# Optimization experiments

Hardware: AMD Instinct MI355X
Metric: run time of the kernel (lower is better)

## Reference

```python
import jax, jax.numpy as jnp
import numpy as np

NQ = 8
NL = 6
DIM = 2 ** NQ
C64 = jnp.complex64
I2 = jnp.eye(2, dtype=C64)
PX = jnp.array([[0., 1.], [1., 0.]], dtype=C64)
PY = jnp.array([[0., -1j], [1j, 0.]], dtype=C64)
PZ = jnp.array([[1., 0.], [0., -1.]], dtype=C64)
# sign of Pauli-Z eigenvalue for each computational basis state, wires 0..3 (wire 0 = MSB)
_idx = np.arange(DIM)
_SIGNS = jnp.asarray(np.stack([1.0 - 2.0 * ((_idx >> (NQ - 1 - w)) & 1) for w in range(4)]).astype(np.float32))  # (4, 256)

def _rot(t, P):
    # exp(-i t/2 P) = cos(t/2) I - i sin(t/2) P
    th = t.astype(jnp.float32) / 2
    return jnp.cos(th) * I2 - 1j * jnp.sin(th) * P

def _apply1(st, U, w):
    # apply 2x2 unitary U on wire w; st: (B, 2,2,...,2)
    s = jnp.moveaxis(st, w + 1, -1)
    return jnp.moveaxis(s @ U.T, -1, w + 1)

def _cnot(st, c, t):
    # flip target axis where control bit == 1
    s = jnp.moveaxis(st, (c + 1, t + 1), (1, 2))
    s = jnp.concatenate([s[:, :1], s[:, 1:, ::-1]], axis=1)
    return jnp.moveaxis(s, (1, 2), (c + 1, t + 1))

def _quantum(x, weights):
    B = x.shape[0]
    # AmplitudeEmbedding with normalize=True
    psi = (x / jnp.linalg.norm(x, axis=1, keepdims=True)).astype(C64)
    st = psi.reshape((B,) + (2,) * NQ)
    for l in range(NL):
        lw = weights[l]
        for q in range(NQ):
            st = _apply1(st, _rot(lw[3 * q], PX), q)
            st = _apply1(st, _rot(lw[3 * q + 1], PY), q)
            st = _apply1(st, _rot(lw[3 * q + 2], PZ), q)
        for i in range(NQ - 1):
            st = _cnot(st, i, i + 1)
        st = _cnot(st, NQ - 1, 0)
        for i in range(0, NQ, 2):
            if i + 2 < NQ:
                st = _cnot(st, i, i + 2)
    probs = jnp.abs(st.reshape(B, DIM)) ** 2
    return probs @ _SIGNS.T  # (B, 4) Z expectations on wires 0..3

def _bn(h, g, b):
    # BatchNorm1d, training mode (batch statistics, biased variance)
    m = h.mean(0)
    v = h.var(0)
    return g * (h - m) * jax.lax.rsqrt(v + 1e-5) + b

def _forward(x, q_weights, aW, ab, fW1, fb1, fW2, fb2, cW1, cb1, g1, be1, cW2, cb2, g2, be2, cW3, cb3, cW4, cb4):
    q = _quantum(x, q_weights)                     # (B, 4)
    qf = q @ aW.T + ab                             # quantum_adapter
    cf = jnp.tanh(jax.nn.relu(x @ fW1.T + fb1) @ fW2.T + fb2)  # feature_processor
    h = qf + cf
    h = jax.nn.relu(_bn(h @ cW1.T + cb1, g1, be1))
    h = jax.nn.relu(_bn(h @ cW2.T + cb2, g2, be2))
    h = jax.nn.relu(h @ cW3.T + cb3)
    return jax.nn.sigmoid(h @ cW4.T + cb4)         # (B, 1)

def setup_inputs():
    key = jax.random.key(0)
    ks = jax.random.split(key, 21)
    f32 = jnp.float32
    r = lambda k, shp, s: jax.random.normal(k, shp, dtype=f32) * s
    B = 8192
    return {
        'x': r(ks[0], (B, 256), 1.0),
        'q_weights': r(ks[1], (NL, NQ * 3), 1.0),
        'aW': r(ks[2], (4, 4), 0.5), 'ab': r(ks[3], (4,), 0.1),
        'fW1': r(ks[4], (64, 256), 0.0625), 'fb1': r(ks[5], (64,), 0.05),
        'fW2': r(ks[6], (4, 64), 0.125), 'fb2': r(ks[7], (4,), 0.05),
        'cW1': r(ks[8], (32, 4), 0.5), 'cb1': r(ks[9], (32,), 0.05),
        'g1': 1.0 + r(ks[10], (32,), 0.05), 'be1': r(ks[11], (32,), 0.05),
        'cW2': r(ks[12], (16, 32), 0.18), 'cb2': r(ks[13], (16,), 0.05),
        'g2': 1.0 + r(ks[14], (16,), 0.05), 'be2': r(ks[15], (16,), 0.05),
        'cW3': r(ks[16], (8, 16), 0.25), 'cb3': r(ks[17], (8,), 0.05),
        'cW4': r(ks[18], (1, 8), 0.35), 'cb4': r(ks[19], (1,), 0.05),
    }

def reference(x, q_weights, aW, ab, fW1, fb1, fW2, fb2, cW1, cb1, g1, be1, cW2, cb2, g2, be2, cW3, cb3, cW4, cb4):
    return _forward(x, q_weights, aW, ab, fW1, fb1, fW2, fb2, cW1, cb1, g1, be1, cW2, cb2, g2, be2, cW3, cb3, cW4, cb4)
```

## Files before the change

### kernel.cpp

```cpp
#include <hip/hip_runtime.h>
#include <math.h>

#define INV_B (1.0f / 8192.0f)

typedef float  v2f  __attribute__((ext_vector_type(2)));
typedef _Float16 half8 __attribute__((ext_vector_type(8)));
typedef float  f32x4 __attribute__((ext_vector_type(4)));

struct QTables {
    int xm[6][8];
    int rm[6][8];
    int meas[4];
};
constexpr QTables make_tables() {
    QTables T{};
    int Mrow[8] = {}, Ncol[8] = {};
    for (int b = 0; b < 8; ++b) { Mrow[b] = 1 << b; Ncol[b] = 1 << b; }
    constexpr int bc[11] = {7,6,5,4,3,2,1,0,7,5,3};
    constexpr int bt[11] = {6,5,4,3,2,1,0,7,5,3,1};
    for (int l = 0; l < 6; ++l) {
        for (int w = 0; w < 8; ++w) { T.xm[l][w] = Ncol[7 - w]; T.rm[l][w] = Mrow[7 - w]; }
        for (int k = 0; k < 11; ++k) { Mrow[bt[k]] ^= Mrow[bc[k]]; Ncol[bc[k]] ^= Ncol[bt[k]]; }
    }
    for (int w = 0; w < 4; ++w) T.meas[w] = Mrow[7 - w];
    return T;
}
constexpr QTables TB = make_tables();

template<int ML>
static __device__ __forceinline__ float lanex(float v) {
    if constexpr (ML == 0) { return v; }
    else if constexpr (ML == 1) { return __int_as_float(__builtin_amdgcn_update_dpp(0, __float_as_int(v), 0xB1, 0xF, 0xF, true)); }
    else if constexpr (ML == 2) { return __int_as_float(__builtin_amdgcn_update_dpp(0, __float_as_int(v), 0x4E, 0xF, 0xF, true)); }
    else if constexpr (ML == 3) { return __int_as_float(__builtin_amdgcn_update_dpp(0, __float_as_int(v), 0x1B, 0xF, 0xF, true)); }
    else if constexpr (ML < 32) { return __int_as_float(__builtin_amdgcn_ds_swizzle(__float_as_int(v), 0x1F | (ML << 10))); }
    else { return __shfl_xor(v, ML, 64); }
}

static __device__ __forceinline__ float tanh_fast(float v) {
    const float c = fminf(fmaxf(v, -10.f), 10.f);
    const float e = __expf(2.f * c);
    return (e - 1.f) / (e + 1.f);
}

template<int XM, int RM>
static __device__ __forceinline__ void gate(v2f (&z)[4], const int lane,
                                            const float u00r, const float u00i,
                                            const float u01r, const float u01i) {
    constexpr int ML = XM >> 2, MR = XM & 3;
    constexpr int RL = RM >> 2, RR = RM & 3;
    const int pl = __popc(lane & RL) & 1;
    const float csi0 = pl ? -u00i : u00i;
    const float cpr0 = pl ? -u01r : u01r;
    const float csi1 = -csi0, cpr1 = -cpr0;
    v2f p[4];
    #pragma unroll
    for (int r = 0; r < 4; ++r) {
        p[r].x = lanex<ML>(z[r ^ MR].x);
        p[r].y = lanex<ML>(z[r ^ MR].y);
    }
    #pragma unroll
    for (int r = 0; r < 4; ++r) {
        const int pb = __builtin_popcount(r & RR) & 1;
        const float csi = pb ? csi1 : csi0;
        const float cpr = pb ? cpr1 : cpr0;
        const v2f zs = { -z[r].y, z[r].x };
        const v2f ps = { -p[r].y, p[r].x };
        z[r] = ((u00r * z[r] + csi * zs) + cpr * p[r]) + u01i * ps;
    }
}

#define XS 264
__global__ __launch_bounds__(256) void k_pre(
        const float* __restrict__ x, const float* __restrict__ qw,
        const float* __restrict__ fW1, const float* __restrict__ fb1,
        const float* __restrict__ fW2, const float* __restrict__ fb2,
        _Float16* __restrict__ Wt, float* __restrict__ cfws,
        float* __restrict__ accz) {
    const int t = threadIdx.x, b = blockIdx.x;

    if (b >= 128) {
        __shared__ float4 Us[48];
        if (t < 48) {
            const int l = t >> 3, q = t & 7;
            const float* a = qw + l * 24 + q * 3;
            const float h1 = 0.5f * a[0], h2 = 0.5f * a[1], h3 = 0.5f * a[2];
            const float c1 = cosf(h1), s1 = sinf(h1);
            const float c2 = cosf(h2), s2 = sinf(h2);
            const float c3 = cosf(h3), s3 = sinf(h3);
            const float m00r =  c1 * c2, m00i =  s1 * s2;
            const float m01r = -c1 * s2, m01i = -s1 * c2;
            float4 u;
            u.x = m00r * c3 + m00i * s3;  u.y = m00i * c3 - m00r * s3;
            u.z = m01r * c3 + m01i * s3;  u.w = m01i * c3 - m01r * s3;
            Us[t] = u;
        }
        __syncthreads();
        const int lane = t & 63, wv = t >> 6;
        const int k = (b - 128) * 4 + wv;
        v2f z[4];
        #pragma unroll
        for (int r = 0; r < 4; ++r) {
            z[r].x = (4 * lane + r == k) ? 1.f : 0.f;
            z[r].y = 0.f;
        }
#define GATE(L, W) { const float4 u = Us[(L) * 8 + (W)]; \
                     gate<TB.xm[L][W], TB.rm[L][W]>(z, lane, u.x, u.y, u.z, u.w); }
#define LAYER(L) GATE(L,0) GATE(L,1) GATE(L,2) GATE(L,3) GATE(L,4) GATE(L,5) GATE(L,6) GATE(L,7)
        LAYER(0) LAYER(1) LAYER(2) LAYER(3) LAYER(4) LAYER(5)
#undef LAYER
#undef GATE
        #pragma unroll
        for (int r = 0; r < 4; ++r) {
            const int i = 4 * lane + r;
            Wt[(long)i * 256 + k]         = (_Float16)z[r].x;
            Wt[(long)(256 + i) * 256 + k] = (_Float16)z[r].y;
        }
        return;
    }

    if (t < 16) accz[b * 16 + t] = 0.f;

    __shared__ _Float16 xl[64 * XS];
    __shared__ _Float16 wl[64 * XS];
    const long r0 = (long)b * 64;
    #pragma unroll
    for (int i = 0; i < 16; ++i) {
        const int idx = i * 256 + t;
        const int row = idx >> 6, c4 = idx & 63;
        const float4 xv = ((const float4*)(x + (r0 + row) * 256))[c4];
        _Float16* d = &xl[row * XS + c4 * 4];
        d[0] = (_Float16)xv.x; d[1] = (_Float16)xv.y;
        d[2] = (_Float16)xv.z; d[3] = (_Float16)xv.w;
        const float4 wv2 = ((const float4*)(fW1 + (long)row * 256))[c4];
        _Float16* e = &wl[row * XS + c4 * 4];
        e[0] = (_Float16)wv2.x; e[1] = (_Float16)wv2.y;
        e[2] = (_Float16)wv2.z; e[3] = (_Float16)wv2.w;
    }
    __syncthreads();

    const int lane = t & 63, w4 = t >> 6;
    const int g = lane >> 4, col = lane & 15;
    const int rloc = w4 * 16 + col;

    half8 bf[8];
    #pragma unroll
    for (int kb = 0; kb < 8; ++kb)
        bf[kb] = *(const half8*)&xl[rloc * XS + kb * 32 + g * 8];

    float accc[4] = {0.f, 0.f, 0.f, 0.f};
    #pragma unroll
    for (int jc = 0; jc < 4; ++jc) {
        f32x4 cv = {0.f, 0.f, 0.f, 0.f};
        #pragma unroll
        for (int kb = 0; kb < 8; ++kb) {
            const half8 af = *(const half8*)&wl[(jc * 16 + col) * XS + kb * 32 + g * 8];
            cv = __builtin_amdgcn_mfma_f32_16x16x32_f16(af, bf[kb], cv, 0, 0, 0);
        }
        #pragma unroll
        for (int r = 0; r < 4; ++r) {
            const int j = jc * 16 + g * 4 + r;
            const float z = fmaxf(cv[r] + fb1[j], 0.f);
            #pragma unroll
            for (int c = 0; c < 4; ++c) accc[c] += z * fW2[c * 64 + j];
        }
    }
    #pragma unroll
    for (int c = 0; c < 4; ++c) {
        accc[c] += __shfl_xor(accc[c], 16, 64);
        accc[c] += __shfl_xor(accc[c], 32, 64);
    }
    if (g == 0) {
        float4 o;
        o.x = tanh_fast(accc[0] + fb2[0]);
        o.y = tanh_fast(accc[1] + fb2[1]);
        o.z = tanh_fast(accc[2] + fb2[2]);
        o.w = tanh_fast(accc[3] + fb2[3]);
        ((float4*)cfws)[r0 + w4 * 16 + col] = o;
    }
}

__global__ __launch_bounds__(128) void k_gemm(
        const float* __restrict__ x, const _Float16* __restrict__ Wt,
        const float* __restrict__ cfws,
        const float* __restrict__ aW, const float* __restrict__ ab,
        float* __restrict__ hws, float* __restrict__ acc1) {
    const int t = threadIdx.x;
    const int lane = t & 63, w = t >> 6;
    const int col = lane & 15, quad = lane >> 4;
    const int R0 = blockIdx.x * 32;

    __shared__ _Float16 xa[32 * XS];
    #pragma unroll
    for (int i = 0; i < 16; ++i) {
        const int idx = i * 128 + t;
        const int row = idx >> 6, c4 = idx & 63;
        const float4 xv = ((const float4*)(x + (long)(R0 + row) * 256))[c4];
        _Float16* d = &xa[row * XS + c4 * 4];
        d[0] = (_Float16)xv.x; d[1] = (_Float16)xv.y;
        d[2] = (_Float16)xv.z; d[3] = (_Float16)xv.w;
    }
    __syncthreads();

    half8 af[8];
    #pragma unroll
    for (int kb = 0; kb < 8; ++kb)
        af[kb] = *(const half8*)&xa[(w * 16 + col) * XS + kb * 32 + quad * 8];

    int slm[4];
    #pragma unroll
    for (int mw = 0; mw < 4; ++mw) slm[mw] = __popc(col & TB.meas[mw]) & 1;

    float sS[4] = {0.f, 0.f, 0.f, 0.f};
    float sq[4][4] = {{0.f}};
    const _Float16* bre = Wt + (long)col * 256;
    const _Float16* bim = Wt + (long)(256 + col) * 256;

    #pragma unroll
    for (int c = 0; c < 16; ++c) {
        f32x4 cr0 = {0.f,0.f,0.f,0.f}, cr1 = {0.f,0.f,0.f,0.f};
        f32x4 ci0 = {0.f,0.f,0.f,0.f}, ci1 = {0.f,0.f,0.f,0.f};
        const long rowoff = (long)(c * 16) * 256 + quad * 8;
        #pragma unroll
        for (int kb = 0; kb < 4; ++kb) {
            const half8 br = *(const half8*)(bre + rowoff + kb * 32);
            cr0 = __builtin_amdgcn_mfma_f32_16x16x32_f16(af[kb], br, cr0, 0, 0, 0);
            const half8 bi = *(const half8*)(bim + rowoff + kb * 32);
            ci0 = __builtin_amdgcn_mfma_f32_16x16x32_f16(af[kb], bi, ci0, 0, 0, 0);
            const half8 br2 = *(const half8*)(bre + rowoff + (kb + 4) * 32);
            cr1 = __builtin_amdgcn_mfma_f32_16x16x32_f16(af[kb + 4], br2, cr1, 0, 0, 0);
            const half8 bi2 = *(const half8*)(bim + rowoff + (kb + 4) * 32);
            ci1 = __builtin_amdgcn_mfma_f32_16x16x32_f16(af[kb + 4], bi2, ci1, 0, 0, 0);
        }
        float sgn[4];
        #pragma unroll
        for (int mw = 0; mw < 4; ++mw) {
            const int scw = __builtin_popcount((c * 16) & TB.meas[mw]) & 1;
            sgn[mw] = (slm[mw] ^ scw) ? -1.f : 1.f;
        }
        #pragma unroll
        for (int r = 0; r < 4; ++r) {
            const float re = cr0[r] + cr1[r], im = ci0[r] + ci1[r];
            const float p = re * re + im * im;
            sS[r] += p;
            #pragma unroll
            for (int mw = 0; mw < 4; ++mw) sq[mw][r] = fmaf(sgn[mw], p, sq[mw][r]);
        }
    }

    #pragma unroll
    for (int r = 0; r < 4; ++r) {
        sS[r] += lanex<1>(sS[r]); sS[r] += lanex<2>(sS[r]);
        sS[r] += lanex<4>(sS[r]); sS[r] += lanex<8>(sS[r]);
        #pragma unroll
        for (int mw = 0; mw < 4; ++mw) {
            sq[mw][r] += lanex<1>(sq[mw][r]); sq[mw][r] += lanex<2>(sq[mw][r]);
            sq[mw][r] += lanex<4>(sq[mw][r]); sq[mw][r] += lanex<8>(sq[mw][r]);
        }
    }

    __shared__ float hb[32][4];
    if (col == 0) {
        #pragma unroll
        for (int r = 0; r < 4; ++r) {
            const int mloc = w * 16 + quad * 4 + r;
            const int row = R0 + mloc;
            const float inv = 1.0f / sS[r];
            float qe[4];
            #pragma unroll
            for (int mw = 0; mw < 4; ++mw) qe[mw] = sq[mw][r] * inv;
            const float4 cfv = ((const float4*)cfws)[row];
            const float cf[4] = {cfv.x, cfv.y, cfv.z, cfv.w};
            float h[4];
            #pragma unroll
            for (int kk = 0; kk < 4; ++kk) {
                float s = ab[kk] + cf[kk];
                #pragma unroll
                for (int j = 0; j < 4; ++j) s += aW[kk * 4 + j] * qe[j];
                h[kk] = s;
            }
            ((float4*)hws)[row] = make_float4(h[0], h[1], h[2], h[3]);
            hb[mloc][0] = h[0]; hb[mloc][1] = h[1];
            hb[mloc][2] = h[2]; hb[mloc][3] = h[3];
        }
    }
    __syncthreads();
    if (t < 20) {
        const int j = (t - 4) >> 2, kk = (t - 4) & 3;
        float v = 0.f;
        for (int rr = 0; rr < 32; ++rr)
            v += (t < 4) ? hb[rr][t] : hb[rr][j] * hb[rr][kk];
        atomicAdd(acc1 + (blockIdx.x & 31) * 20 + t, v);
    }
}

__global__ __launch_bounds__(64) void k_mid(
        const float* __restrict__ hws, const float* __restrict__ acc1,
        const float* __restrict__ cW1, const float* __restrict__ cb1,
        const float* __restrict__ g1, const float* __restrict__ be1,
        const float* __restrict__ cW2, const float* __restrict__ cb2,
        float* __restrict__ z2ws, float* __restrict__ acc2) {
    const int t = threadIdx.x;
    __shared__ float sA[20];
    __shared__ float m1s[32], is1[32];
    if (t < 20) {
        float s = 0.f;
        for (int sl = 0; sl < 32; ++sl) s += acc1[sl * 20 + t];
        sA[t] = s;
    }
    __syncthreads();
    if (t < 32) {
        float mu[4], w[4];
        #pragma unroll
        for (int k = 0; k < 4; ++k) mu[k] = sA[k] * INV_B;
        float m = cb1[t];
        #pragma unroll
        for (int k = 0; k < 4; ++k) { w[k] = cW1[t * 4 + k]; m += w[k] * mu[k]; }
        float var = 0.f;
        #pragma unroll
        for (int a2 = 0; a2 < 4; ++a2)
            #pragma unroll
            for (int b2 = 0; b2 < 4; ++b2)
                var += w[a2] * w[b2] * (sA[4 + a2 * 4 + b2] * INV_B - mu[a2] * mu[b2]);
        m1s[t] = m;
        is1[t] = 1.0f / sqrtf(var + 1e-5f);
    }
    __syncthreads();

    const long e = (long)blockIdx.x * 64 + t;
    const float4 h4 = ((const float4*)hws)[e];
    const float h[4] = {h4.x, h4.y, h4.z, h4.w};
    float a1[32];
    #pragma unroll
    for (int j = 0; j < 32; ++j) {
        float zz = cb1[j];
        #pragma unroll
        for (int k = 0; k < 4; ++k) zz += cW1[j * 4 + k] * h[k];
        a1[j] = fmaxf((zz - m1s[j]) * is1[j] * g1[j] + be1[j], 0.f);
    }
    float z2[16];
    #pragma unroll
    for (int k = 0; k < 16; ++k) {
        float s = cb2[k];
        #pragma unroll
        for (int j = 0; j < 32; ++j) s += cW2[k * 32 + j] * a1[j];
        z2[k] = s;
    }
    float4* zp = (float4*)(z2ws + e * 16);
    zp[0] = make_float4(z2[0], z2[1], z2[2], z2[3]);
    zp[1] = make_float4(z2[4], z2[5], z2[6], z2[7]);
    zp[2] = make_float4(z2[8], z2[9], z2[10], z2[11]);
    zp[3] = make_float4(z2[12], z2[13], z2[14], z2[15]);

    float sv[16], sq2[16];
    #pragma unroll
    for (int k = 0; k < 16; ++k) { sv[k] = z2[k]; sq2[k] = z2[k] * z2[k]; }
    #pragma unroll
    for (int m = 1; m < 64; m <<= 1) {
        #pragma unroll
        for (int k = 0; k < 16; ++k) {
            sv[k] += __shfl_xor(sv[k], m, 64);
            sq2[k] += __shfl_xor(sq2[k], m, 64);
        }
    }
    if (t == 0) {
        float* dst = acc2 + ((int)blockIdx.x & 31) * 32;
        #pragma unroll
        for (int k = 0; k < 16; ++k) atomicAdd(dst + k, sv[k]);
        #pragma unroll
        for (int k = 0; k < 16; ++k) atomicAdd(dst + 16 + k, sq2[k]);
    }
}

__global__ __launch_bounds__(64) void k_out(
        const float* __restrict__ z2ws, const float* __restrict__ acc2,
        const float* __restrict__ g2, const float* __restrict__ be2,
        const float* __restrict__ cW3, const float* __restrict__ cb3,
        const float* __restrict__ cW4, const float* __restrict__ cb4,
        float* __restrict__ out) {
    const int t = threadIdx.x;
    __shared__ float sB[32];
    __shared__ float m2s[16], is2[16];
    if (t < 32) {
        float s = 0.f;
        for (int sl = 0; sl < 32; ++sl) s += acc2[sl * 32 + t];
        sB[t] = s;
    }
    __syncthreads();
    if (t < 16) {
        const float m = sB[t] * INV_B;
        const float var = sB[16 + t] * INV_B - m * m;
        m2s[t] = m;
        is2[t] = 1.0f / sqrtf(var + 1e-5f);
    }
    __syncthreads();

    const long e = (long)blockIdx.x * 64 + t;
    const float4* zp = (const float4*)(z2ws + e * 16);
    const float4 v0 = zp[0], v1 = zp[1], v2 = zp[2], v3 = zp[3];
    const float z2[16] = {v0.x, v0.y, v0.z, v0.w, v1.x, v1.y, v1.z, v1.w,
                          v2.x, v2.y, v2.z, v2.w, v3.x, v3.y, v3.z, v3.w};
    float a2[16];
    #pragma unroll
    for (int k = 0; k < 16; ++k)
        a2[k] = fmaxf((z2[k] - m2s[k]) * is2[k] * g2[k] + be2[k], 0.f);
    float z3[8];
    #pragma unroll
    for (int j = 0; j < 8; ++j) {
        float s = cb3[j];
        #pragma unroll
        for (int k = 0; k < 16; ++k) s += cW3[j * 16 + k] * a2[k];
        z3[j] = fmaxf(s, 0.f);
    }
    float y = cb4[0];
    #pragma unroll
    for (int j = 0; j < 8; ++j) y += cW4[j] * z3[j];
    out[e] = 1.0f / (1.0f + expf(-y));
}

extern "C" void kernel_launch(void* const* d_in, const int* in_sizes, int n_in,
                              void* d_out, int out_size, void* d_ws, size_t ws_size,
                              hipStream_t stream) {
    (void)in_sizes; (void)n_in; (void)out_size; (void)ws_size;
    const float* x   = (const float*)d_in[0];
    const float* qw  = (const float*)d_in[1];
    const float* aW  = (const float*)d_in[2];
    const float* ab  = (const float*)d_in[3];
    const float* fW1 = (const float*)d_in[4];
    const float* fb1 = (const float*)d_in[5];
    const float* fW2 = (const float*)d_in[6];
    const float* fb2 = (const float*)d_in[7];
    const float* cW1 = (const float*)d_in[8];
    const float* cb1 = (const float*)d_in[9];
    const float* g1  = (const float*)d_in[10];
    const float* be1 = (const float*)d_in[11];
    const float* cW2 = (const float*)d_in[12];
    const float* cb2 = (const float*)d_in[13];
    const float* g2  = (const float*)d_in[14];
    const float* be2 = (const float*)d_in[15];
    const float* cW3 = (const float*)d_in[16];
    const float* cb3 = (const float*)d_in[17];
    const float* cW4 = (const float*)d_in[18];
    const float* cb4 = (const float*)d_in[19];

    float* ws   = (float*)d_ws;
    float* acc1 = ws;
    float* acc2 = ws + 1024;
    float* cfws = ws + 4096;
    float* hws  = ws + 40960;
    float* z2ws = ws + 81920;
    _Float16* Wt = (_Float16*)(ws + 215040);

    k_pre <<<192, 256, 0, stream>>>(x, qw, fW1, fb1, fW2, fb2, Wt, cfws, ws);
    k_gemm<<<256, 128, 0, stream>>>(x, Wt, cfws, aW, ab, hws, acc1);
    k_mid <<<128, 64, 0, stream>>>(hws, acc1, cW1, cb1, g1, be1, cW2, cb2, z2ws, acc2);
    k_out <<<128, 64, 0, stream>>>(z2ws, acc2, g2, be2, cW3, cb3, cW4, cb4, (float*)d_out);
}
```

Before: 137.7 us.

## Fuse feature MLP into quantum GEMM and merge tail kernels via grid barrier

The classical feature MLP (x·fW1, relu, fW2, tanh) moves out of the prelude kernel and into the main GEMM kernel, which reuses the fp16 x fragments already staged in LDS. The prelude now only builds the circuit unitary and an fp16 copy of fW1, so the second read of x and the cf workspace round-trip go away. The mid and output kernels are merged into one kernel that uses an atomic counter spin-barrier for the second BatchNorm statistics, dropping the z2 workspace and one launch. The spin barrier assumes all 128 blocks are resident at once, and the counter is zeroed only by the prelude's accumulator clear.

```diff
diff --git a/kernel.cpp b/kernel.cpp
--- a/kernel.cpp
+++ b/kernel.cpp
@@ -70,119 +70,59 @@
     }
 }
 
-#define XS 264
 __global__ __launch_bounds__(256) void k_pre(
-        const float* __restrict__ x, const float* __restrict__ qw,
-        const float* __restrict__ fW1, const float* __restrict__ fb1,
-        const float* __restrict__ fW2, const float* __restrict__ fb2,
-        _Float16* __restrict__ Wt, float* __restrict__ cfws,
+        const float* __restrict__ qw, const float* __restrict__ fW1,
+        _Float16* __restrict__ Wt, _Float16* __restrict__ fW1h,
         float* __restrict__ accz) {
     const int t = threadIdx.x, b = blockIdx.x;
-
-    if (b >= 128) {
-        __shared__ float4 Us[48];
-        if (t < 48) {
-            const int l = t >> 3, q = t & 7;
-            const float* a = qw + l * 24 + q * 3;
-            const float h1 = 0.5f * a[0], h2 = 0.5f * a[1], h3 = 0.5f * a[2];
-            const float c1 = cosf(h1), s1 = sinf(h1);
-            const float c2 = cosf(h2), s2 = sinf(h2);
-            const float c3 = cosf(h3), s3 = sinf(h3);
-            const float m00r =  c1 * c2, m00i =  s1 * s2;
-            const float m01r = -c1 * s2, m01i = -s1 * c2;
-            float4 u;
-            u.x = m00r * c3 + m00i * s3;  u.y = m00i * c3 - m00r * s3;
-            u.z = m01r * c3 + m01i * s3;  u.w = m01i * c3 - m01r * s3;
-            Us[t] = u;
-        }
-        __syncthreads();
-        const int lane = t & 63, wv = t >> 6;
-        const int k = (b - 128) * 4 + wv;
-        v2f z[4];
-        #pragma unroll
-        for (int r = 0; r < 4; ++r) {
-            z[r].x = (4 * lane + r == k) ? 1.f : 0.f;
-            z[r].y = 0.f;
-        }
+    const int e = b * 256 + t;
+    fW1h[e] = (_Float16)fW1[e];
+    if (t < 32) accz[b * 32 + t] = 0.f;
+
+    __shared__ float4 Us[48];
+    if (t < 48) {
+        const int l = t >> 3, q = t & 7;
+        const float* a = qw + l * 24 + q * 3;
+        const float h1 = 0.5f * a[0], h2 = 0.5f * a[1], h3 = 0.5f * a[2];
+        const float c1 = cosf(h1), s1 = sinf(h1);
+        const float c2 = cosf(h2), s2 = sinf(h2);
+        const float c3 = cosf(h3), s3 = sinf(h3);
+        const float m00r =  c1 * c2, m00i =  s1 * s2;
+        const float m01r = -c1 * s2, m01i = -s1 * c2;
+        float4 u;
+        u.x = m00r * c3 + m00i * s3;  u.y = m00i * c3 - m00r * s3;
+        u.z = m01r * c3 + m01i * s3;  u.w = m01i * c3 - m01r * s3;
+        Us[t] = u;
+    }
+    __syncthreads();
+    const int lane = t & 63, wv = t >> 6;
+    const int k = b * 4 + wv;
+    v2f z[4];
+    #pragma unroll
+    for (int r = 0; r < 4; ++r) {
+        z[r].x = (4 * lane + r == k) ? 1.f : 0.f;
+        z[r].y = 0.f;
+    }
 #define GATE(L, W) { const float4 u = Us[(L) * 8 + (W)]; \
                      gate<TB.xm[L][W], TB.rm[L][W]>(z, lane, u.x, u.y, u.z, u.w); }
 #define LAYER(L) GATE(L,0) GATE(L,1) GATE(L,2) GATE(L,3) GATE(L,4) GATE(L,5) GATE(L,6) GATE(L,7)
-        LAYER(0) LAYER(1) LAYER(2) LAYER(3) LAYER(4) LAYER(5)
+    LAYER(0) LAYER(1) LAYER(2) LAYER(3) LAYER(4) LAYER(5)
 #undef LAYER
 #undef GATE
-        #pragma unroll
-        for (int r = 0; r < 4; ++r) {
-            const int i = 4 * lane + r;
-            Wt[(long)i * 256 + k]         = (_Float16)z[r].x;
-            Wt[(long)(256 + i) * 256 + k] = (_Float16)z[r].y;
-        }
-        return;
-    }
-
-    if (t < 16) accz[b * 16 + t] = 0.f;
-
-    __shared__ _Float16 xl[64 * XS];
-    __shared__ _Float16 wl[64 * XS];
-    const long r0 = (long)b * 64;
-    #pragma unroll
-    for (int i = 0; i < 16; ++i) {
-        const int idx = i * 256 + t;
-        const int row = idx >> 6, c4 = idx & 63;
-        const float4 xv = ((const float4*)(x + (r0 + row) * 256))[c4];
-        _Float16* d = &xl[row * XS + c4 * 4];
-        d[0] = (_Float16)xv.x; d[1] = (_Float16)xv.y;
-        d[2] = (_Float16)xv.z; d[3] = (_Float16)xv.w;
-        const float4 wv2 = ((const float4*)(fW1 + (long)row * 256))[c4];
-        _Float16* e = &wl[row * XS + c4 * 4];
-        e[0] = (_Float16)wv2.x; e[1] = (_Float16)wv2.y;
-        e[2] = (_Float16)wv2.z; e[3] = (_Float16)wv2.w;
-    }
-    __syncthreads();
-
-    const int lane = t & 63, w4 = t >> 6;
-    const int g = lane >> 4, col = lane & 15;
-    const int rloc = w4 * 16 + col;
-
-    half8 bf[8];
-    #pragma unroll
-    for (int kb = 0; kb < 8; ++kb)
-        bf[kb] = *(const half8*)&xl[rloc * XS + kb * 32 + g * 8];
-
-    float accc[4] = {0.f, 0.f, 0.f, 0.f};
-    #pragma unroll
-    for (int jc = 0; jc < 4; ++jc) {
-        f32x4 cv = {0.f, 0.f, 0.f, 0.f};
-        #pragma unroll
-        for (int kb = 0; kb < 8; ++kb) {
-            const half8 af = *(const half8*)&wl[(jc * 16 + col) * XS + kb * 32 + g * 8];
-            cv = __builtin_amdgcn_mfma_f32_16x16x32_f16(af, bf[kb], cv, 0, 0, 0);
-        }
-        #pragma unroll
-        for (int r = 0; r < 4; ++r) {
-            const int j = jc * 16 + g * 4 + r;
-            const float z = fmaxf(cv[r] + fb1[j], 0.f);
-            #pragma unroll
-            for (int c = 0; c < 4; ++c) accc[c] += z * fW2[c * 64 + j];
-        }
-    }
-    #pragma unroll
-    for (int c = 0; c < 4; ++c) {
-        accc[c] += __shfl_xor(accc[c], 16, 64);
-        accc[c] += __shfl_xor(accc[c], 32, 64);
-    }
-    if (g == 0) {
-        float4 o;
-        o.x = tanh_fast(accc[0] + fb2[0]);
-        o.y = tanh_fast(accc[1] + fb2[1]);
-        o.z = tanh_fast(accc[2] + fb2[2]);
-        o.w = tanh_fast(accc[3] + fb2[3]);
-        ((float4*)cfws)[r0 + w4 * 16 + col] = o;
-    }
-}
-
+    #pragma unroll
+    for (int r = 0; r < 4; ++r) {
+        const int i = 4 * lane + r;
+        Wt[(long)i * 256 + k]         = (_Float16)z[r].x;
+        Wt[(long)(256 + i) * 256 + k] = (_Float16)z[r].y;
+    }
+}
+
+#define XS 264
 __global__ __launch_bounds__(128) void k_gemm(
         const float* __restrict__ x, const _Float16* __restrict__ Wt,
-        const float* __restrict__ cfws,
+        const _Float16* __restrict__ fW1h,
+        const float* __restrict__ fb1, const float* __restrict__ fW2,
+        const float* __restrict__ fb2,
         const float* __restrict__ aW, const float* __restrict__ ab,
         float* __restrict__ hws, float* __restrict__ acc1) {
     const int t = threadIdx.x;
@@ -206,6 +146,36 @@
     #pragma unroll
     for (int kb = 0; kb < 8; ++kb)
         af[kb] = *(const half8*)&xa[(w * 16 + col) * XS + kb * 32 + quad * 8];
+
+    float sc[4][4] = {{0.f}};
+    #pragma unroll
+    for (int jt = 0; jt < 4; ++jt) {
+        const int j = jt * 16 + col;
+        f32x4 mv = {0.f, 0.f, 0.f, 0.f};
+        #pragma unroll
+        for (int kb = 0; kb < 8; ++kb) {
+            const half8 bw = *(const half8*)(fW1h + (long)j * 256 + kb * 32 + quad * 8);
+            mv = __builtin_amdgcn_mfma_f32_16x16x32_f16(af[kb], bw, mv, 0, 0, 0);
+        }
+        const float b1 = fb1[j];
+        const float w20 = fW2[j], w21 = fW2[64 + j];
+        const float w22 = fW2[128 + j], w23 = fW2[192 + j];
+        #pragma unroll
+        for (int r = 0; r < 4; ++r) {
+            const float z1 = fmaxf(mv[r] + b1, 0.f);
+            sc[0][r] = fmaf(z1, w20, sc[0][r]);
+            sc[1][r] = fmaf(z1, w21, sc[1][r]);
+            sc[2][r] = fmaf(z1, w22, sc[2][r]);
+            sc[3][r] = fmaf(z1, w23, sc[3][r]);
+        }
+    }
+    #pragma unroll
+    for (int c = 0; c < 4; ++c)
+        #pragma unroll
+        for (int r = 0; r < 4; ++r) {
+            sc[c][r] += lanex<1>(sc[c][r]); sc[c][r] += lanex<2>(sc[c][r]);
+            sc[c][r] += lanex<4>(sc[c][r]); sc[c][r] += lanex<8>(sc[c][r]);
+        }
 
     int slm[4];
     #pragma unroll
@@ -247,7 +217,6 @@
             for (int mw = 0; mw < 4; ++mw) sq[mw][r] = fmaf(sgn[mw], p, sq[mw][r]);
         }
     }
-
     #pragma unroll
     for (int r = 0; r < 4; ++r) {
         sS[r] += lanex<1>(sS[r]); sS[r] += lanex<2>(sS[r]);
@@ -266,11 +235,11 @@
             const int mloc = w * 16 + quad * 4 + r;
             const int row = R0 + mloc;
             const float inv = 1.0f / sS[r];
-            float qe[4];
+            float qe[4], cf[4];
             #pragma unroll
             for (int mw = 0; mw < 4; ++mw) qe[mw] = sq[mw][r] * inv;
-            const float4 cfv = ((const float4*)cfws)[row];
-            const float cf[4] = {cfv.x, cfv.y, cfv.z, cfv.w};
+            #pragma unroll
+            for (int c = 0; c < 4; ++c) cf[c] = tanh_fast(sc[c][r] + fb2[c]);
             float h[4];
             #pragma unroll
             for (int kk = 0; kk < 4; ++kk) {
@@ -294,15 +263,19 @@
     }
 }
 
-__global__ __launch_bounds__(64) void k_mid(
+__global__ __launch_bounds__(64) void k_tail(
         const float* __restrict__ hws, const float* __restrict__ acc1,
         const float* __restrict__ cW1, const float* __restrict__ cb1,
         const float* __restrict__ g1, const float* __restrict__ be1,
         const float* __restrict__ cW2, const float* __restrict__ cb2,
-        float* __restrict__ z2ws, float* __restrict__ acc2) {
+        const float* __restrict__ g2, const float* __restrict__ be2,
+        const float* __restrict__ cW3, const float* __restrict__ cb3,
+        const float* __restrict__ cW4, const float* __restrict__ cb4,
+        float* __restrict__ acc2, int* __restrict__ cnt,
+        float* __restrict__ out) {
     const int t = threadIdx.x;
-    __shared__ float sA[20];
-    __shared__ float m1s[32], is1[32];
+    __shared__ float sA[20], m1s[32], is1[32];
+    __shared__ float sB[32], m2s[16], is2[16];
     if (t < 20) {
         float s = 0.f;
         for (int sl = 0; sl < 32; ++sl) s += acc1[sl * 20 + t];
@@ -346,11 +319,6 @@
         for (int j = 0; j < 32; ++j) s += cW2[k * 32 + j] * a1[j];
         z2[k] = s;
     }
-    float4* zp = (float4*)(z2ws + e * 16);
-    zp[0] = make_float4(z2[0], z2[1], z2[2], z2[3]);
-    zp[1] = make_float4(z2[4], z2[5], z2[6], z2[7]);
-    zp[2] = make_float4(z2[8], z2[9], z2[10], z2[11]);
-    zp[3] = make_float4(z2[12], z2[13], z2[14], z2[15]);
 
     float sv[16], sq2[16];
     #pragma unroll
@@ -369,37 +337,28 @@
         for (int k = 0; k < 16; ++k) atomicAdd(dst + k, sv[k]);
         #pragma unroll
         for (int k = 0; k < 16; ++k) atomicAdd(dst + 16 + k, sq2[k]);
-    }
-}
-
-__global__ __launch_bounds__(64) void k_out(
-        const float* __restrict__ z2ws, const float* __restrict__ acc2,
-        const float* __restrict__ g2, const float* __restrict__ be2,
-        const float* __restrict__ cW3, const float* __restrict__ cb3,
-        const float* __restrict__ cW4, const float* __restrict__ cb4,
-        float* __restrict__ out) {
-    const int t = threadIdx.x;
-    __shared__ float sB[32];
-    __shared__ float m2s[16], is2[16];
+        __threadfence();
+        __hip_atomic_fetch_add(cnt, 1, __ATOMIC_ACQ_REL, __HIP_MEMORY_SCOPE_AGENT);
+        while (__hip_atomic_load(cnt, __ATOMIC_ACQUIRE, __HIP_MEMORY_SCOPE_AGENT)
+               < (int)gridDim.x) { __builtin_amdgcn_s_sleep(2); }
+    }
+    __syncthreads();
+
     if (t < 32) {
         float s = 0.f;
-        for (int sl = 0; sl < 32; ++sl) s += acc2[sl * 32 + t];
+        for (int sl = 0; sl < 32; ++sl)
+            s += __hip_atomic_load(acc2 + sl * 32 + t, __ATOMIC_RELAXED,
+                                   __HIP_MEMORY_SCOPE_AGENT);
         sB[t] = s;
     }
     __syncthreads();
     if (t < 16) {
         const float m = sB[t] * INV_B;
-        const float var = sB[16 + t] * INV_B - m * m;
         m2s[t] = m;
-        is2[t] = 1.0f / sqrtf(var + 1e-5f);
-    }
-    __syncthreads();
-
-    const long e = (long)blockIdx.x * 64 + t;
-    const float4* zp = (const float4*)(z2ws + e * 16);
-    const float4 v0 = zp[0], v1 = zp[1], v2 = zp[2], v3 = zp[3];
-    const float z2[16] = {v0.x, v0.y, v0.z, v0.w, v1.x, v1.y, v1.z, v1.w,
-                          v2.x, v2.y, v2.z, v2.w, v3.x, v3.y, v3.z, v3.w};
+        is2[t] = 1.0f / sqrtf(sB[16 + t] * INV_B - m * m + 1e-5f);
+    }
+    __syncthreads();
+
     float a2[16];
     #pragma unroll
     for (int k = 0; k < 16; ++k)
@@ -445,14 +404,15 @@
 
     float* ws   = (float*)d_ws;
     float* acc1 = ws;
+    int*   cnt  = (int*)(ws + 640);
     float* acc2 = ws + 1024;
-    float* cfws = ws + 4096;
-    float* hws  = ws + 40960;
-    float* z2ws = ws + 81920;
-    _Float16* Wt = (_Float16*)(ws + 215040);
-
-    k_pre <<<192, 256, 0, stream>>>(x, qw, fW1, fb1, fW2, fb2, Wt, cfws, ws);
-    k_gemm<<<256, 128, 0, stream>>>(x, Wt, cfws, aW, ab, hws, acc1);
-    k_mid <<<128, 64, 0, stream>>>(hws, acc1, cW1, cb1, g1, be1, cW2, cb2, z2ws, acc2);
-    k_out <<<128, 64, 0, stream>>>(z2ws, acc2, g2, be2, cW3, cb3, cW4, cb4, (float*)d_out);
-}
+    float* hws  = ws + 4096;
+    _Float16* Wt   = (_Float16*)(ws + 40960);
+    _Float16* fW1h = (_Float16*)(ws + 110592);
+
+    k_pre <<<64, 256, 0, stream>>>(qw, fW1, Wt, fW1h, ws);
+    k_gemm<<<256, 128, 0, stream>>>(x, Wt, fW1h, fb1, fW2, fb2, aW, ab, hws, acc1);
+    k_tail<<<128, 64, 0, stream>>>(hws, acc1, cW1, cb1, g1, be1, cW2, cb2,
+                                   g2, be2, cW3, cb3, cW4, cb4, acc2, cnt,
+                                   (float*)d_out);
+}
```

Result: slower. 143.8 us (+4.4%).
